# Kernel tuning notes

Hardware: AMD Instinct MI355X
Metric: run time of the kernel (lower is better)

The kernel has to match this reference:

```python
import jax, jax.numpy as jnp
import numpy as np

N = 20000      # n_nodes
E = 320000     # n_edges (multiple of 4, so _from_coo drops nothing)
D = 512        # embed_dim
H = 8          # num_heads
DK = D // H    # d_k = 64


def setup_inputs() -> dict:
    key = jax.random.key(0)
    ks = jax.random.split(key, 12)
    x = jax.random.normal(ks[0], (N, D), jnp.float32)
    rows = jnp.sort(jax.random.randint(ks[1], (E,), 0, N))
    cols = jax.random.randint(ks[2], (E,), 0, N)
    edge_index = jnp.stack([rows, cols]).astype(jnp.int32)  # [2, E]
    att_bias = jax.random.normal(ks[3], (E, H), jnp.float32)
    s = float(1.0 / np.sqrt(D))  # ~xavier scale
    Wq = jax.random.normal(ks[4], (D, D), jnp.float32) * s
    Wk = jax.random.normal(ks[5], (D, D), jnp.float32) * s
    Wv = jax.random.normal(ks[6], (D, D), jnp.float32) * s
    Wo = jax.random.normal(ks[7], (D, D), jnp.float32) * s
    bq = jnp.zeros((D,), jnp.float32)
    bk = jnp.zeros((D,), jnp.float32)
    bv = jnp.zeros((D,), jnp.float32)
    bo = jnp.zeros((D,), jnp.float32)
    return dict(x=x, edge_index=edge_index, att_bias=att_bias,
                Wq=Wq, bq=bq, Wk=Wk, bk=bk, Wv=Wv, bv=bv, Wo=Wo, bo=bo)


def reference(x, edge_index, att_bias, Wq, bq, Wk, bk, Wv, bv, Wo, bo):
    n = x.shape[0]
    rows, cols = edge_index[0], edge_index[1]
    # per-head projections: [n, H, DK]
    q = (x @ Wq + bq).reshape(n, H, DK)
    k = (x @ Wk + bk).reshape(n, H, DK)
    v = (x @ Wv + bv).reshape(n, H, DK)
    scale = 1.0 / jnp.sqrt(jnp.asarray(DK, x.dtype))
    # masked QK^T on the edge pattern, plus additive bias: [E, H]
    logits = jnp.einsum('ehd,ehd->eh', q[rows] * scale, k[cols]) + att_bias
    # CSR (segment) softmax over each destination row
    row_max = jax.ops.segment_max(logits, rows, num_segments=n)      # [n, H]
    p = jnp.exp(logits - row_max[rows])                              # [E, H]
    denom = jax.ops.segment_sum(p, rows, num_segments=n)            # [n, H]
    att = p / denom[rows]                                            # [E, H]
    # sparse-dense bmm: y[i] = sum_{e: rows[e]=i} att[e] * v[cols[e]]
    y = jax.ops.segment_sum(att[:, :, None] * v[cols], rows, num_segments=n)  # [n, H, DK]
    out = y.reshape(n, H * DK) @ Wo + bo
    return out
```

## Files before the change

### kernel.cpp

```cpp
#include <hip/hip_runtime.h>
#include <hip/hip_bf16.h>

typedef unsigned short ushort_t;
typedef unsigned int uint32;
typedef __attribute__((ext_vector_type(8))) short short8;
typedef __attribute__((ext_vector_type(4))) float floatx4;

#define DEV __device__ __forceinline__

DEV float b2f(ushort_t u) { return __uint_as_float(((uint32)u) << 16); }
DEV ushort_t f2b(float f) {
  __hip_bfloat16 h = __float2bfloat16(f);
  return __builtin_bit_cast(unsigned short, h);
}
DEV void unpack8(const uint4& u, float* f) {
  f[0] = __uint_as_float(u.x << 16); f[1] = __uint_as_float(u.x & 0xffff0000u);
  f[2] = __uint_as_float(u.y << 16); f[3] = __uint_as_float(u.y & 0xffff0000u);
  f[4] = __uint_as_float(u.z << 16); f[5] = __uint_as_float(u.z & 0xffff0000u);
  f[6] = __uint_as_float(u.w << 16); f[7] = __uint_as_float(u.w & 0xffff0000u);
}

#define GLOAD_LDS(gp, lp) \
  __builtin_amdgcn_global_load_lds((const __attribute__((address_space(1))) uint32*)(gp), \
                                   (__attribute__((address_space(3))) uint32*)(lp), 16, 0, 0)

__global__ __launch_bounds__(256) void k_detect(const ushort_t* __restrict__ x,
                                                int* __restrict__ flag) {
  __shared__ int red[256];
  int tid = threadIdx.x;
  int wild = 0;
  for (int i = tid; i < 4096; i += 256) {
    uint32 e = (x[i] >> 7) & 0xFFu;
    if (e < 100u || e > 140u) wild++;
  }
  red[tid] = wild;
  __syncthreads();
  for (int s = 128; s > 0; s >>= 1) {
    if (tid < s) red[tid] += red[tid + s];
    __syncthreads();
  }
  if (tid == 0) flag[0] = (red[0] > 400) ? 1 : 0;
}

__global__ __launch_bounds__(256) void k_transpose(
    const void* __restrict__ Wq, const void* __restrict__ Wk,
    const void* __restrict__ Wv, const void* __restrict__ Wo,
    ushort_t* __restrict__ WT4, const int* __restrict__ flagp) {
  __shared__ ushort_t t[32][33];
  int isf32 = *flagp;
  int z = blockIdx.z;
  const void* src = (z == 0) ? Wq : (z == 1) ? Wk : (z == 2) ? Wv : Wo;
  ushort_t* dst = WT4 + (size_t)z * 512 * 512;
  int bx = blockIdx.x, by = blockIdx.y;
  int tx = threadIdx.x, ty = threadIdx.y;
#pragma unroll
  for (int i = 0; i < 4; i++) {
    size_t idx = (size_t)(by * 32 + ty + 8 * i) * 512 + bx * 32 + tx;
    ushort_t v = isf32 ? f2b(((const float*)src)[idx]) : ((const ushort_t*)src)[idx];
    t[ty + 8 * i][tx] = v;
  }
  __syncthreads();
#pragma unroll
  for (int i = 0; i < 4; i++)
    dst[(size_t)(bx * 32 + ty + 8 * i) * 512 + by * 32 + tx] = t[tx][ty + 8 * i];
}

__global__ __launch_bounds__(256) void k_biases(
    const void* __restrict__ bq, const void* __restrict__ bk,
    const void* __restrict__ bv, const void* __restrict__ bo,
    float* __restrict__ biasf, const int* __restrict__ flagp) {
  int i = blockIdx.x * 256 + threadIdx.x;
  if (i >= 2048) return;
  int z = i >> 9, j = i & 511;
  const void* b = (z == 0) ? bq : (z == 1) ? bk : (z == 2) ? bv : bo;
  biasf[i] = (*flagp) ? ((const float*)b)[j] : b2f(((const ushort_t*)b)[j]);
}

__global__ __launch_bounds__(256) void k_convx(
    const void* __restrict__ x, ushort_t* __restrict__ xb, int n8,
    const int* __restrict__ flagp) {
  int i = blockIdx.x * 256 + threadIdx.x;
  if (i >= n8) return;
  if (*flagp) {
    const float* xf = (const float*)x + (size_t)i * 8;
    float4 f0 = ((const float4*)xf)[0];
    float4 f1 = ((const float4*)xf)[1];
    uint4 o;
    o.x = (uint32)f2b(f0.x) | ((uint32)f2b(f0.y) << 16);
    o.y = (uint32)f2b(f0.z) | ((uint32)f2b(f0.w) << 16);
    o.z = (uint32)f2b(f1.x) | ((uint32)f2b(f1.y) << 16);
    o.w = (uint32)f2b(f1.z) | ((uint32)f2b(f1.w) << 16);
    ((uint4*)xb)[i] = o;
  } else {
    ((uint4*)xb)[i] = ((const uint4*)x)[i];
  }
}

__global__ void k_build_rp(const int* __restrict__ rows, int E, int N, int* __restrict__ rp) {
  int i = blockIdx.x * blockDim.x + threadIdx.x;
  if (i > N) return;
  int lo = 0, hi = E;
  while (lo < hi) {
    int mid = (lo + hi) >> 1;
    if (rows[mid] < i) lo = mid + 1; else hi = mid;
  }
  rp[i] = lo;
}

DEV void gemm_body(const ushort_t* __restrict__ A, const ushort_t* __restrict__ BT,
                   const float* __restrict__ bias, void* C,
                   int M, int ldc, float scale, int row0, int by, int f32out) {
  __shared__ ushort_t As[128 * 32];
  __shared__ ushort_t Bs[128 * 32];
  int tid = threadIdx.x;
  int w = tid >> 6, lane = tid & 63;
  int sr = lane >> 2;
  int sk = (lane & 3) * 8;

  floatx4 acc[4][4];
#pragma unroll
  for (int i = 0; i < 4; i++)
#pragma unroll
    for (int j = 0; j < 4; j++)
#pragma unroll
      for (int r = 0; r < 4; r++) acc[i][j][r] = 0.f;

  int lm = lane & 15, quad = lane >> 4;
  int wr = w >> 1, wc = w & 1;
  const int nG = by * 128 + w * 32;

  int rA0 = row0 + w * 32 + sr; if (rA0 >= M) rA0 = M - 1;
  int rA1 = rA0 + 16;          if (rA1 >= M) rA1 = M - 1;
  const ushort_t* gA0 = A + (size_t)rA0 * 512 + sk;
  const ushort_t* gA1 = A + (size_t)rA1 * 512 + sk;
  const ushort_t* gB0 = BT + (size_t)(nG + sr) * 512 + sk;
  const ushort_t* gB1 = BT + (size_t)(nG + 16 + sr) * 512 + sk;

  for (int k0 = 0; k0 < 512; k0 += 32) {
    GLOAD_LDS(gA0 + k0, As + (w * 32 + 0) * 32);
    GLOAD_LDS(gA1 + k0, As + (w * 32 + 16) * 32);
    GLOAD_LDS(gB0 + k0, Bs + (w * 32 + 0) * 32);
    GLOAD_LDS(gB1 + k0, Bs + (w * 32 + 16) * 32);
    __syncthreads();

    const ushort_t* pa = As + (wr * 64 + lm) * 32 + quad * 8;
    const ushort_t* pb = Bs + (wc * 64 + lm) * 32 + quad * 8;
    short8 af[4], bfr[4];
#pragma unroll
    for (int t4 = 0; t4 < 4; t4++) {
      af[t4]  = *(const short8*)(pa + t4 * 16 * 32);
      bfr[t4] = *(const short8*)(pb + t4 * 16 * 32);
    }
#pragma unroll
    for (int mt = 0; mt < 4; mt++)
#pragma unroll
      for (int nt = 0; nt < 4; nt++)
        acc[mt][nt] = __builtin_amdgcn_mfma_f32_16x16x32_bf16(af[mt], bfr[nt], acc[mt][nt], 0, 0, 0);
    __syncthreads();
  }

  int colB = by * 128 + wc * 64 + lm;
  float bv4[4];
#pragma unroll
  for (int nt = 0; nt < 4; nt++) bv4[nt] = bias[colB + nt * 16];
#pragma unroll
  for (int mt = 0; mt < 4; mt++) {
    int rg0 = row0 + wr * 64 + mt * 16 + quad * 4;
#pragma unroll
    for (int nt = 0; nt < 4; nt++) {
#pragma unroll
      for (int r = 0; r < 4; r++) {
        int rg = rg0 + r;
        if (rg < M) {
          float val = (acc[mt][nt][r] + bv4[nt]) * scale;
          size_t off = (size_t)rg * ldc + colB + nt * 16;
          if (f32out) ((float*)C)[off] = val;
          else        ((ushort_t*)C)[off] = f2b(val);
        }
      }
    }
  }
}

__global__ __launch_bounds__(256) void k_gemm_qkv(
    const ushort_t* __restrict__ xb, const ushort_t* __restrict__ WT4,
    const float* __restrict__ biasf, ushort_t* Qp, ushort_t* KV, int M) {
  int z = blockIdx.z;
  const ushort_t* BT = WT4 + (size_t)z * 512 * 512;
  const float* bias = biasf + (size_t)z * 512;
  ushort_t* Cp = (z == 0) ? Qp : (z == 1) ? KV : (KV + 512);
  int ldc = (z == 0) ? 512 : 1024;
  float scale = (z == 0) ? 0.125f : 1.0f;
  gemm_body(xb, BT, bias, Cp, M, ldc, scale, blockIdx.x * 128, blockIdx.y, 0);
}

__global__ __launch_bounds__(256) void k_gemm_out(
    const ushort_t* __restrict__ y, const ushort_t* __restrict__ WT4,
    const float* __restrict__ biasf, void* out, int M,
    const int* __restrict__ flagp) {
  gemm_body(y, WT4 + (size_t)3 * 512 * 512, biasf + 3 * 512, out, M, 512, 1.0f,
            blockIdx.x * 128, blockIdx.y, *flagp);
}

__global__ __launch_bounds__(256) void k_edge(
    ushort_t* Qy, const ushort_t* __restrict__ KV,
    const void* __restrict__ ab, const int* __restrict__ cols,
    const int* __restrict__ rp, int Nn, int E, const int* __restrict__ flagp) {
  int node = blockIdx.x * 4 + (threadIdx.x >> 6);
  if (node >= Nn) return;
  int lane = threadIdx.x & 63;
  int h8 = lane >> 3;
  int isf32 = *flagp;

  uint4 qu = ((const uint4*)(Qy + (size_t)node * 512))[lane];
  float qf[8];
  unpack8(qu, qf);

  int e0 = rp[node], e1 = rp[node + 1];
  if (e0 < 0) e0 = 0;
  if (e1 > E) e1 = E;

  float m = -__builtin_inff(), s = 0.f;
  float accv[8];
#pragma unroll
  for (int j = 0; j < 8; j++) accv[j] = 0.f;

  uint4 ku0, vu0, ku1, vu1;
  float ab0, ab1;
  if (e0 < e1) {
    int c = cols[e0];
    const ushort_t* kvrow = KV + (size_t)c * 1024;
    ku0 = ((const uint4*)kvrow)[lane];
    vu0 = ((const uint4*)(kvrow + 512))[lane];
    size_t bi = (size_t)e0 * 8 + h8;
    ab0 = isf32 ? ((const float*)ab)[bi] : b2f(((const ushort_t*)ab)[bi]);
  }

  for (int e = e0; e < e1; ++e) {
    if (e + 1 < e1) {
      int c = cols[e + 1];
      const ushort_t* kvrow = KV + (size_t)c * 1024;
      ku1 = ((const uint4*)kvrow)[lane];
      vu1 = ((const uint4*)(kvrow + 512))[lane];
      size_t bi = (size_t)(e + 1) * 8 + h8;
      ab1 = isf32 ? ((const float*)ab)[bi] : b2f(((const ushort_t*)ab)[bi]);
    }
    float kf[8];
    unpack8(ku0, kf);
    float d = 0.f;
#pragma unroll
    for (int j = 0; j < 8; j++) d = fmaf(qf[j], kf[j], d);
    d += __shfl_xor(d, 1);
    d += __shfl_xor(d, 2);
    d += __shfl_xor(d, 4);
    float logit = d + ab0;
    float mn = fmaxf(m, logit);
    float alpha = __expf(m - mn);
    float pw = __expf(logit - mn);
    s = s * alpha + pw;
    float vf[8];
    unpack8(vu0, vf);
#pragma unroll
    for (int j = 0; j < 8; j++) accv[j] = accv[j] * alpha + pw * vf[j];
    m = mn;
    ku0 = ku1; vu0 = vu1; ab0 = ab1;
  }

  float inv = (e1 > e0 && s > 0.f) ? 1.f / s : 0.f;
  ushort_t hb[8];
#pragma unroll
  for (int j = 0; j < 8; j++) hb[j] = f2b(accv[j] * inv);
  uint4 uh;
  uh.x = (uint32)hb[0] | ((uint32)hb[1] << 16);
  uh.y = (uint32)hb[2] | ((uint32)hb[3] << 16);
  uh.z = (uint32)hb[4] | ((uint32)hb[5] << 16);
  uh.w = (uint32)hb[6] | ((uint32)hb[7] << 16);
  ((uint4*)(Qy + (size_t)node * 512))[lane] = uh;
}

extern "C" void kernel_launch(void* const* d_in, const int* in_sizes, int n_in,
                              void* d_out, int out_size, void* d_ws, size_t ws_size,
                              hipStream_t stream) {
  const void* x  = d_in[0];
  const int* ei  = (const int*)d_in[1];
  const void* ab = d_in[2];
  const void* Wq = d_in[3];
  const void* bq = d_in[4];
  const void* Wk = d_in[5];
  const void* bk = d_in[6];
  const void* Wv = d_in[7];
  const void* bv = d_in[8];
  const void* Wo = d_in[9];
  const void* bo = d_in[10];

  const int D = 512;
  int M = in_sizes[0] / D;
  int E = in_sizes[1] / 2;
  const int* rows = ei;
  const int* cols = ei + E;

  char* p = (char*)d_ws;
  size_t off = 0;
  auto carve = [&](size_t bytes) -> void* {
    off = (off + 255) & ~(size_t)255;
    void* r = p + off;
    off += bytes;
    return r;
  };
  int* flag      = (int*)carve(4);
  ushort_t* WT4  = (ushort_t*)carve((size_t)4 * 512 * 512 * 2);
  float* biasf   = (float*)carve((size_t)4 * 512 * 4);
  ushort_t* xb   = (ushort_t*)carve((size_t)M * 512 * 2);
  ushort_t* Qp   = (ushort_t*)carve((size_t)M * 512 * 2);
  ushort_t* KV   = (ushort_t*)carve((size_t)M * 1024 * 2);
  int* rp        = (int*)carve((size_t)(M + 1) * 4);
  (void)ws_size;

  k_detect<<<1, 256, 0, stream>>>((const ushort_t*)x, flag);
  k_transpose<<<dim3(16, 16, 4), dim3(32, 8), 0, stream>>>(Wq, Wk, Wv, Wo, WT4, flag);
  k_biases<<<8, 256, 0, stream>>>(bq, bk, bv, bo, biasf, flag);
  int n8 = M * 512 / 8;
  k_convx<<<(n8 + 255) / 256, 256, 0, stream>>>(x, xb, n8, flag);
  k_build_rp<<<(M + 1 + 255) / 256, 256, 0, stream>>>(rows, E, M, rp);

  int rb = (M + 127) / 128;
  k_gemm_qkv<<<dim3(rb, 4, 3), 256, 0, stream>>>(xb, WT4, biasf, Qp, KV, M);
  k_edge<<<(M + 3) / 4, 256, 0, stream>>>(Qp, KV, ab, cols, rp, M, E, flag);
  k_gemm_out<<<dim3(rb, 4, 1), 256, 0, stream>>>(Qp, WT4, biasf, d_out, M, flag);
}
```

Before: 313.6 us.

## Deepen edge prefetch to four slots and drop online-softmax max tracking

```diff
diff --git a/kernel.cpp b/kernel.cpp
--- a/kernel.cpp
+++ b/kernel.cpp
@@ -217,59 +217,60 @@
   unpack8(qu, qf);
 
   int e0 = rp[node], e1 = rp[node + 1];
-  if (e0 < 0) e0 = 0;
-  if (e1 > E) e1 = E;
-
-  float m = -__builtin_inff(), s = 0.f;
-  float accv[8];
-#pragma unroll
-  for (int j = 0; j < 8; j++) accv[j] = 0.f;
-
-  uint4 ku0, vu0, ku1, vu1;
-  float ab0, ab1;
-  if (e0 < e1) {
-    int c = cols[e0];
+  int cnt = e1 - e0;
+
+  float s0 = 0.f, s1 = 0.f;
+  float acc0[8], acc1[8];
+#pragma unroll
+  for (int j = 0; j < 8; j++) { acc0[j] = 0.f; acc1[j] = 0.f; }
+
+  uint4 kb[4], vb[4];
+  float abf[4];
+
+  auto pref = [&](int t, int slot) {
+    int valid = t < cnt;
+    int ei = valid ? (e0 + t) : e0;
+    int c = valid ? cols[ei] : 0;
     const ushort_t* kvrow = KV + (size_t)c * 1024;
-    ku0 = ((const uint4*)kvrow)[lane];
-    vu0 = ((const uint4*)(kvrow + 512))[lane];
-    size_t bi = (size_t)e0 * 8 + h8;
-    ab0 = isf32 ? ((const float*)ab)[bi] : b2f(((const ushort_t*)ab)[bi]);
-  }
-
-  for (int e = e0; e < e1; ++e) {
-    if (e + 1 < e1) {
-      int c = cols[e + 1];
-      const ushort_t* kvrow = KV + (size_t)c * 1024;
-      ku1 = ((const uint4*)kvrow)[lane];
-      vu1 = ((const uint4*)(kvrow + 512))[lane];
-      size_t bi = (size_t)(e + 1) * 8 + h8;
-      ab1 = isf32 ? ((const float*)ab)[bi] : b2f(((const ushort_t*)ab)[bi]);
-    }
+    kb[slot] = ((const uint4*)kvrow)[lane];
+    vb[slot] = ((const uint4*)(kvrow + 512))[lane];
+    size_t bi = (size_t)ei * 8 + h8;
+    float a = isf32 ? ((const float*)ab)[bi] : b2f(((const ushort_t*)ab)[bi]);
+    abf[slot] = valid ? a : -1e30f;
+  };
+  auto consume = [&](int slot, float* acc, float& s) {
     float kf[8];
-    unpack8(ku0, kf);
+    unpack8(kb[slot], kf);
     float d = 0.f;
 #pragma unroll
     for (int j = 0; j < 8; j++) d = fmaf(qf[j], kf[j], d);
     d += __shfl_xor(d, 1);
     d += __shfl_xor(d, 2);
     d += __shfl_xor(d, 4);
-    float logit = d + ab0;
-    float mn = fmaxf(m, logit);
-    float alpha = __expf(m - mn);
-    float pw = __expf(logit - mn);
-    s = s * alpha + pw;
+    float logit = fminf(d + abf[slot], 80.f);
+    float pw = __expf(logit);
+    s += pw;
     float vf[8];
-    unpack8(vu0, vf);
-#pragma unroll
-    for (int j = 0; j < 8; j++) accv[j] = accv[j] * alpha + pw * vf[j];
-    m = mn;
-    ku0 = ku1; vu0 = vu1; ab0 = ab1;
-  }
-
-  float inv = (e1 > e0 && s > 0.f) ? 1.f / s : 0.f;
+    unpack8(vb[slot], vf);
+#pragma unroll
+    for (int j = 0; j < 8; j++) acc[j] = fmaf(pw, vf[j], acc[j]);
+  };
+
+  pref(0, 0); pref(1, 1); pref(2, 2); pref(3, 3);
+  int iters = (cnt + 3) >> 2;
+  for (int it = 0; it < iters; ++it) {
+    int nt = it * 4 + 4;
+    consume(0, acc0, s0); pref(nt + 0, 0);
+    consume(1, acc1, s1); pref(nt + 1, 1);
+    consume(2, acc0, s0); pref(nt + 2, 2);
+    consume(3, acc1, s1); pref(nt + 3, 3);
+  }
+
+  float s = s0 + s1;
+  float inv = (cnt > 0 && s > 0.f) ? 1.f / s : 0.f;
   ushort_t hb[8];
 #pragma unroll
-  for (int j = 0; j < 8; j++) hb[j] = f2b(accv[j] * inv);
+  for (int j = 0; j < 8; j++) hb[j] = f2b((acc0[j] + acc1[j]) * inv);
   uint4 uh;
   uh.x = (uint32)hb[0] | ((uint32)hb[1] << 16);
   uh.y = (uint32)hb[2] | ((uint32)hb[3] << 16);
```

Result: no change. 315.4 us (+0.6%).
